# Kernel tuning notes

Hardware: AMD Instinct MI355X
Metric: run time of the kernel (lower is better)

Reference implementation:

```python
import jax, jax.numpy as jnp
import numpy as np

EPS = 1e-10


def setup_inputs() -> dict:
    key = jax.random.key(0)
    k1, k2, k3 = jax.random.split(key, 3)
    B, K, M, X, Y = 32, 4, 3, 256, 256
    predictions = jax.random.uniform(k1, (B, K, X, Y), dtype=jnp.float32)
    inputs = jax.random.normal(k2, (B, M, X, Y), dtype=jnp.float32)
    heart = jax.random.randint(k3, (B, 1, X, Y), 0, 2, dtype=jnp.int32)
    return {"predictions": predictions, "inputs": inputs, "heart": heart}


def reference(predictions, inputs, heart):
    # predictions: [B,K,X,Y] soft class maps; inputs: [B,M,X,Y]; heart: [B,1,X,Y] 0/1 ROI
    mask = (heart[:, 0] == 1).astype(predictions.dtype)            # [B,X,Y]
    n = jnp.sum(mask, axis=(-2, -1))                                # [B] masked pixel count
    pred = predictions * mask[:, None]                              # [B,K,X,Y] zero outside ROI
    # alpha[b,k] = mean of pred over masked pixels
    alpha = jnp.sum(pred, axis=(-2, -1)) / n[:, None]               # [B,K]
    s = jnp.sum(pred, axis=(-2, -1)) + EPS                          # [B,K]
    # weighted means mu[b,k,m] = sum(pred*inp)/ (sum(pred)+eps)
    mu = jnp.einsum('bkxy,bmxy->bkm', pred, inputs) / s[:, :, None]  # [B,K,M]
    diff = inputs[:, None] - mu[:, :, :, None, None]                 # [B,K,M,X,Y]
    var = jnp.einsum('bkmxy,bkxy->bkm', diff * diff, pred) / s[:, :, None] + EPS  # [B,K,M]
    # Gaussian pdf per (k,m), product over channels m (done in log-space, same math)
    v = var[:, :, :, None, None]
    log_pdf = -0.5 * jnp.log(2.0 * jnp.pi * v) - (diff * diff) / (2.0 * v)  # [B,K,M,X,Y]
    g = jnp.exp(jnp.sum(log_pdf, axis=2))                            # [B,K,X,Y] = prod_m pdf
    mix = jnp.sum(alpha[:, :, None, None] * g, axis=1)               # [B,X,Y]
    ll = jnp.log(mix + EPS)                                          # [B,X,Y]
    # mean of -log-likelihood over masked pixels per batch, then mean over batch
    per_b = -jnp.sum(mask * ll, axis=(-2, -1)) / n                   # [B]
    return jnp.mean(per_b)
```

## Files before the change

kernel.cpp:

```cpp
#include <hip/hip_runtime.h>

#define EPSF 1e-10f

constexpr int B = 32, K = 4, M = 3;
constexpr int NPIX = 256 * 256;
constexpr int BLOCKS_PER_B = 32;
constexpr int THREADS = 256;
constexpr int WAVES = THREADS / 64;
constexpr int CHUNKS = NPIX / (BLOCKS_PER_B * THREADS * 4);
constexpr int NVALS = 1 + K + 2 * K * M;

constexpr int OFF_PART1 = 0;
constexpr int OFF_PART2 = OFF_PART1 + B * BLOCKS_PER_B * NVALS;
constexpr int OFF_ALPHA = OFF_PART2 + B * BLOCKS_PER_B;
constexpr int OFF_MU    = OFF_ALPHA + B * K;
constexpr int OFF_IV    = OFF_MU + B * K * M;
constexpr int OFF_CST   = OFF_IV + B * K * M;
constexpr int OFF_NOUT  = OFF_CST + B * K;

__device__ __forceinline__ float wave_reduce(float v) {
    #pragma unroll
    for (int off = 32; off > 0; off >>= 1) v += __shfl_down(v, off, 64);
    return v;
}

__global__ __launch_bounds__(THREADS) void pass1_kernel(
    const float* __restrict__ pred, const float* __restrict__ xin,
    const int* __restrict__ heart, float* __restrict__ ws) {
    const int b  = blockIdx.x / BLOCKS_PER_B;
    const int cb = blockIdx.x % BLOCKS_PER_B;

    float nacc = 0.0f;
    float Wk[K] = {};
    float Pa[K][M] = {};
    float Qa[K][M] = {};

    #pragma unroll
    for (int it = 0; it < CHUNKS; ++it) {
        const int p0 = (((cb * CHUNKS + it) * THREADS) + threadIdx.x) * 4;

        const int4 h4 = *(const int4*)(heart + b * NPIX + p0);
        float mk[4];
        mk[0] = (h4.x == 1) ? 1.0f : 0.0f;
        mk[1] = (h4.y == 1) ? 1.0f : 0.0f;
        mk[2] = (h4.z == 1) ? 1.0f : 0.0f;
        mk[3] = (h4.w == 1) ? 1.0f : 0.0f;
        nacc += (mk[0] + mk[1]) + (mk[2] + mk[3]);

        float xv[M][4];
        #pragma unroll
        for (int m = 0; m < M; ++m) {
            float4 t = *(const float4*)(xin + (b * M + m) * NPIX + p0);
            xv[m][0] = t.x; xv[m][1] = t.y; xv[m][2] = t.z; xv[m][3] = t.w;
        }

        #pragma unroll
        for (int k = 0; k < K; ++k) {
            float4 pr = *(const float4*)(pred + (b * K + k) * NPIX + p0);
            float pm[4];
            pm[0] = pr.x * mk[0]; pm[1] = pr.y * mk[1];
            pm[2] = pr.z * mk[2]; pm[3] = pr.w * mk[3];
            Wk[k] += (pm[0] + pm[1]) + (pm[2] + pm[3]);
            #pragma unroll
            for (int m = 0; m < M; ++m) {
                #pragma unroll
                for (int j = 0; j < 4; ++j) {
                    float px = pm[j] * xv[m][j];
                    Pa[k][m] += px;
                    Qa[k][m] += px * xv[m][j];
                }
            }
        }
    }

    float vals[NVALS];
    vals[0] = nacc;
    #pragma unroll
    for (int k = 0; k < K; ++k) vals[1 + k] = Wk[k];
    #pragma unroll
    for (int k = 0; k < K; ++k)
        #pragma unroll
        for (int m = 0; m < M; ++m) {
            vals[1 + K + k * M + m]         = Pa[k][m];
            vals[1 + K + K * M + k * M + m] = Qa[k][m];
        }

    __shared__ float red[WAVES * NVALS];
    #pragma unroll
    for (int i = 0; i < NVALS; ++i) vals[i] = wave_reduce(vals[i]);
    const int wave = threadIdx.x >> 6;
    if ((threadIdx.x & 63) == 0) {
        #pragma unroll
        for (int i = 0; i < NVALS; ++i) red[wave * NVALS + i] = vals[i];
    }
    __syncthreads();
    const int i = threadIdx.x;
    if (i < NVALS) {
        float s = red[i];
        #pragma unroll
        for (int w = 1; w < WAVES; ++w) s += red[w * NVALS + i];
        ws[OFF_PART1 + (b * BLOCKS_PER_B + cb) * NVALS + i] = s;
    }
}

__global__ __launch_bounds__(B * K) void params_kernel(float* __restrict__ ws) {
    const int t = threadIdx.x;
    const int b = t / K;
    const int k = t % K;

    float n = 0.0f, W = 0.0f, P[M] = {}, Q[M] = {};
    for (int p = 0; p < BLOCKS_PER_B; ++p) {
        const float* base = ws + OFF_PART1 + (b * BLOCKS_PER_B + p) * NVALS;
        n += base[0];
        W += base[1 + k];
        #pragma unroll
        for (int m = 0; m < M; ++m) {
            P[m] += base[1 + K + k * M + m];
            Q[m] += base[1 + K + K * M + k * M + m];
        }
    }

    const float s = W + EPSF;
    ws[OFF_ALPHA + t] = W / n;
    if (k == 0) ws[OFF_NOUT + b] = n;
    float cst = 0.0f;
    #pragma unroll
    for (int m = 0; m < M; ++m) {
        const float mu = P[m] / s;
        const float var = (Q[m] - 2.0f * mu * P[m] + mu * mu * W) / s + EPSF;
        ws[OFF_MU + t * M + m] = mu;
        ws[OFF_IV + t * M + m] = 0.5f / var;
        cst -= 0.5f * logf(6.2831853071795864f * var);
    }
    ws[OFF_CST + t] = cst;
}

__global__ __launch_bounds__(THREADS) void pass2_kernel(
    const float* __restrict__ xin, const int* __restrict__ heart,
    float* __restrict__ ws) {
    const int b  = blockIdx.x / BLOCKS_PER_B;
    const int cb = blockIdx.x % BLOCKS_PER_B;

    float alpha[K], cst[K], mu[K][M], iv[K][M];
    #pragma unroll
    for (int k = 0; k < K; ++k) {
        alpha[k] = ws[OFF_ALPHA + b * K + k];
        cst[k]   = ws[OFF_CST + b * K + k];
        #pragma unroll
        for (int m = 0; m < M; ++m) {
            mu[k][m] = ws[OFF_MU + (b * K + k) * M + m];
            iv[k][m] = ws[OFF_IV + (b * K + k) * M + m];
        }
    }

    float acc = 0.0f;
    #pragma unroll
    for (int it = 0; it < CHUNKS; ++it) {
        const int p0 = (((cb * CHUNKS + it) * THREADS) + threadIdx.x) * 4;

        const int4 h4 = *(const int4*)(heart + b * NPIX + p0);
        int hv[4] = {h4.x, h4.y, h4.z, h4.w};

        float xv[M][4];
        #pragma unroll
        for (int m = 0; m < M; ++m) {
            float4 t = *(const float4*)(xin + (b * M + m) * NPIX + p0);
            xv[m][0] = t.x; xv[m][1] = t.y; xv[m][2] = t.z; xv[m][3] = t.w;
        }

        #pragma unroll
        for (int j = 0; j < 4; ++j) {
            float mix = EPSF;
            #pragma unroll
            for (int k = 0; k < K; ++k) {
                float lp = cst[k];
                #pragma unroll
                for (int m = 0; m < M; ++m) {
                    float d = xv[m][j] - mu[k][m];
                    lp -= d * d * iv[k][m];
                }
                mix += alpha[k] * __expf(lp);
            }
            float mask = (hv[j] == 1) ? 1.0f : 0.0f;
            acc += mask * __logf(mix);
        }
    }

    __shared__ float red[WAVES];
    acc = wave_reduce(acc);
    const int wave = threadIdx.x >> 6;
    if ((threadIdx.x & 63) == 0) red[wave] = acc;
    __syncthreads();
    if (threadIdx.x == 0) {
        float s = red[0];
        #pragma unroll
        for (int w = 1; w < WAVES; ++w) s += red[w];
        ws[OFF_PART2 + b * BLOCKS_PER_B + cb] = s;
    }
}

__global__ __launch_bounds__(64) void final_kernel(const float* __restrict__ ws,
                                                   float* __restrict__ out) {
    const int t = threadIdx.x;
    float val = 0.0f;
    if (t < B) {
        float s = 0.0f;
        for (int p = 0; p < BLOCKS_PER_B; ++p)
            s += ws[OFF_PART2 + t * BLOCKS_PER_B + p];
        val = -s / ws[OFF_NOUT + t];
    }
    val = wave_reduce(val);
    if (t == 0) out[0] = val / (float)B;
}

extern "C" void kernel_launch(void* const* d_in, const int* in_sizes, int n_in,
                              void* d_out, int out_size, void* d_ws, size_t ws_size,
                              hipStream_t stream) {
    const float* pred  = (const float*)d_in[0];
    const float* xin   = (const float*)d_in[1];
    const int*   heart = (const int*)d_in[2];
    float* out = (float*)d_out;
    float* ws  = (float*)d_ws;

    pass1_kernel<<<B * BLOCKS_PER_B, THREADS, 0, stream>>>(pred, xin, heart, ws);
    params_kernel<<<1, B * K, 0, stream>>>(ws);
    pass2_kernel<<<B * BLOCKS_PER_B, THREADS, 0, stream>>>(xin, heart, ws);
    final_kernel<<<1, 64, 0, stream>>>(ws, out);
}
```

Baseline: 113.3 us.

## Fuse all passes into one cooperative kernel with grid syncs and LDS-cached inputs

Replaces the four-kernel sequence with a single cooperative kernel that uses grid-wide syncs between the statistics pass, the per-batch parameter computation and the likelihood pass. Each block keeps its slice of inputs and the mask in shared memory (about 32 KB), so the second pass no longer re-reads inputs and heart from global memory. Every block redundantly reduces the per-batch partials to compute its own parameters, which removes the separate params and final launches. The cost is two grid barriers, higher LDS use that can limit occupancy for 1024 co-resident blocks, and a fallback to the old kernels if the cooperative launch fails.

```diff
diff --git a/kernel.cpp b/kernel.cpp
--- a/kernel.cpp
+++ b/kernel.cpp
@@ -1,22 +1,27 @@
 #include <hip/hip_runtime.h>
+#include <hip/hip_cooperative_groups.h>
+
+namespace cg = cooperative_groups;
 
 #define EPSF 1e-10f
 
 constexpr int B = 32, K = 4, M = 3;
 constexpr int NPIX = 256 * 256;
-constexpr int BLOCKS_PER_B = 32;
+constexpr int BPB = 32;
 constexpr int THREADS = 256;
 constexpr int WAVES = THREADS / 64;
-constexpr int CHUNKS = NPIX / (BLOCKS_PER_B * THREADS * 4);
+constexpr int PXB = NPIX / BPB;
+constexpr int CHUNKS = PXB / (THREADS * 4);
 constexpr int NVALS = 1 + K + 2 * K * M;
-
-constexpr int OFF_PART1 = 0;
-constexpr int OFF_PART2 = OFF_PART1 + B * BLOCKS_PER_B * NVALS;
-constexpr int OFF_ALPHA = OFF_PART2 + B * BLOCKS_PER_B;
+constexpr int PSTRIDE = 32;
+
+constexpr int OFF_P1 = 0;
+constexpr int OFF_LLP = OFF_P1 + B * BPB * PSTRIDE;
+constexpr int OFF_N  = OFF_LLP + B * BPB;
+constexpr int OFF_ALPHA = OFF_N + B;
 constexpr int OFF_MU    = OFF_ALPHA + B * K;
 constexpr int OFF_IV    = OFF_MU + B * K * M;
 constexpr int OFF_CST   = OFF_IV + B * K * M;
-constexpr int OFF_NOUT  = OFF_CST + B * K;
 
 __device__ __forceinline__ float wave_reduce(float v) {
     #pragma unroll
@@ -24,11 +29,17 @@
     return v;
 }
 
-__global__ __launch_bounds__(THREADS) void pass1_kernel(
+__global__ __launch_bounds__(THREADS, 4) void fused_kernel(
     const float* __restrict__ pred, const float* __restrict__ xin,
-    const int* __restrict__ heart, float* __restrict__ ws) {
-    const int b  = blockIdx.x / BLOCKS_PER_B;
-    const int cb = blockIdx.x % BLOCKS_PER_B;
+    const int* __restrict__ heart, float* __restrict__ ws, float* __restrict__ out) {
+    __shared__ float xs[M][PXB];
+    __shared__ float msk[PXB];
+    __shared__ float red[WAVES * NVALS];
+    __shared__ float par[K * 8];
+
+    const int b  = blockIdx.x / BPB;
+    const int cb = blockIdx.x % BPB;
+    const int tid = threadIdx.x;
 
     float nacc = 0.0f;
     float Wk[K] = {};
@@ -37,7 +48,8 @@
 
     #pragma unroll
     for (int it = 0; it < CHUNKS; ++it) {
-        const int p0 = (((cb * CHUNKS + it) * THREADS) + threadIdx.x) * 4;
+        const int li = (it * THREADS + tid) * 4;
+        const int p0 = cb * PXB + li;
 
         const int4 h4 = *(const int4*)(heart + b * NPIX + p0);
         float mk[4];
@@ -45,12 +57,14 @@
         mk[1] = (h4.y == 1) ? 1.0f : 0.0f;
         mk[2] = (h4.z == 1) ? 1.0f : 0.0f;
         mk[3] = (h4.w == 1) ? 1.0f : 0.0f;
+        *(float4*)&msk[li] = make_float4(mk[0], mk[1], mk[2], mk[3]);
         nacc += (mk[0] + mk[1]) + (mk[2] + mk[3]);
 
         float xv[M][4];
         #pragma unroll
         for (int m = 0; m < M; ++m) {
             float4 t = *(const float4*)(xin + (b * M + m) * NPIX + p0);
+            *(float4*)&xs[m][li] = t;
             xv[m][0] = t.x; xv[m][1] = t.y; xv[m][2] = t.z; xv[m][3] = t.w;
         }
 
@@ -84,90 +98,76 @@
             vals[1 + K + k * M + m]         = Pa[k][m];
             vals[1 + K + K * M + k * M + m] = Qa[k][m];
         }
-
-    __shared__ float red[WAVES * NVALS];
     #pragma unroll
     for (int i = 0; i < NVALS; ++i) vals[i] = wave_reduce(vals[i]);
-    const int wave = threadIdx.x >> 6;
-    if ((threadIdx.x & 63) == 0) {
+    const int wave = tid >> 6;
+    if ((tid & 63) == 0) {
         #pragma unroll
         for (int i = 0; i < NVALS; ++i) red[wave * NVALS + i] = vals[i];
     }
     __syncthreads();
-    const int i = threadIdx.x;
-    if (i < NVALS) {
-        float s = red[i];
-        #pragma unroll
-        for (int w = 1; w < WAVES; ++w) s += red[w * NVALS + i];
-        ws[OFF_PART1 + (b * BLOCKS_PER_B + cb) * NVALS + i] = s;
-    }
-}
-
-__global__ __launch_bounds__(B * K) void params_kernel(float* __restrict__ ws) {
-    const int t = threadIdx.x;
-    const int b = t / K;
-    const int k = t % K;
-
-    float n = 0.0f, W = 0.0f, P[M] = {}, Q[M] = {};
-    for (int p = 0; p < BLOCKS_PER_B; ++p) {
-        const float* base = ws + OFF_PART1 + (b * BLOCKS_PER_B + p) * NVALS;
-        n += base[0];
-        W += base[1 + k];
-        #pragma unroll
-        for (int m = 0; m < M; ++m) {
-            P[m] += base[1 + K + k * M + m];
-            Q[m] += base[1 + K + K * M + k * M + m];
-        }
-    }
-
-    const float s = W + EPSF;
-    ws[OFF_ALPHA + t] = W / n;
-    if (k == 0) ws[OFF_NOUT + b] = n;
-    float cst = 0.0f;
-    #pragma unroll
-    for (int m = 0; m < M; ++m) {
-        const float mu = P[m] / s;
-        const float var = (Q[m] - 2.0f * mu * P[m] + mu * mu * W) / s + EPSF;
-        ws[OFF_MU + t * M + m] = mu;
-        ws[OFF_IV + t * M + m] = 0.5f / var;
-        cst -= 0.5f * logf(6.2831853071795864f * var);
-    }
-    ws[OFF_CST + t] = cst;
-}
-
-__global__ __launch_bounds__(THREADS) void pass2_kernel(
-    const float* __restrict__ xin, const int* __restrict__ heart,
-    float* __restrict__ ws) {
-    const int b  = blockIdx.x / BLOCKS_PER_B;
-    const int cb = blockIdx.x % BLOCKS_PER_B;
+    if (tid < NVALS) {
+        float s = red[tid];
+        #pragma unroll
+        for (int w = 1; w < WAVES; ++w) s += red[w * NVALS + tid];
+        ws[OFF_P1 + (b * BPB + cb) * PSTRIDE + tid] = s;
+    }
+    __threadfence();
+    cg::this_grid().sync();
+
+    if (tid < K) {
+        const int k = tid;
+        float n = 0.0f, W = 0.0f, P[M] = {}, Q[M] = {};
+        for (int p = 0; p < BPB; ++p) {
+            const float* base = ws + OFF_P1 + (b * BPB + p) * PSTRIDE;
+            n += base[0];
+            W += base[1 + k];
+            #pragma unroll
+            for (int m = 0; m < M; ++m) {
+                P[m] += base[1 + K + k * M + m];
+                Q[m] += base[1 + K + K * M + k * M + m];
+            }
+        }
+        const float s = W + EPSF;
+        par[k * 8 + 0] = W / n;
+        float cst = 0.0f;
+        #pragma unroll
+        for (int m = 0; m < M; ++m) {
+            const float mu = P[m] / s;
+            const float var = (Q[m] - 2.0f * mu * P[m] + mu * mu * W) / s + EPSF;
+            par[k * 8 + 2 + m] = mu;
+            par[k * 8 + 5 + m] = 0.5f / var;
+            cst -= 0.5f * logf(6.2831853071795864f * var);
+        }
+        par[k * 8 + 1] = cst;
+        if (k == 0 && cb == 0) ws[OFF_N + b] = n;
+    }
+    __syncthreads();
 
     float alpha[K], cst[K], mu[K][M], iv[K][M];
     #pragma unroll
     for (int k = 0; k < K; ++k) {
-        alpha[k] = ws[OFF_ALPHA + b * K + k];
-        cst[k]   = ws[OFF_CST + b * K + k];
-        #pragma unroll
-        for (int m = 0; m < M; ++m) {
-            mu[k][m] = ws[OFF_MU + (b * K + k) * M + m];
-            iv[k][m] = ws[OFF_IV + (b * K + k) * M + m];
+        alpha[k] = par[k * 8 + 0];
+        cst[k]   = par[k * 8 + 1];
+        #pragma unroll
+        for (int m = 0; m < M; ++m) {
+            mu[k][m] = par[k * 8 + 2 + m];
+            iv[k][m] = par[k * 8 + 5 + m];
         }
     }
 
     float acc = 0.0f;
     #pragma unroll
     for (int it = 0; it < CHUNKS; ++it) {
-        const int p0 = (((cb * CHUNKS + it) * THREADS) + threadIdx.x) * 4;
-
-        const int4 h4 = *(const int4*)(heart + b * NPIX + p0);
-        int hv[4] = {h4.x, h4.y, h4.z, h4.w};
-
+        const int li = (it * THREADS + tid) * 4;
+        const float4 mk4 = *(const float4*)&msk[li];
+        const float mk[4] = {mk4.x, mk4.y, mk4.z, mk4.w};
         float xv[M][4];
         #pragma unroll
         for (int m = 0; m < M; ++m) {
-            float4 t = *(const float4*)(xin + (b * M + m) * NPIX + p0);
+            float4 t = *(const float4*)&xs[m][li];
             xv[m][0] = t.x; xv[m][1] = t.y; xv[m][2] = t.z; xv[m][3] = t.w;
         }
-
         #pragma unroll
         for (int j = 0; j < 4; ++j) {
             float mix = EPSF;
@@ -181,11 +181,179 @@
                 }
                 mix += alpha[k] * __expf(lp);
             }
-            float mask = (hv[j] == 1) ? 1.0f : 0.0f;
-            acc += mask * __logf(mix);
-        }
-    }
-
+            acc += mk[j] * __logf(mix);
+        }
+    }
+
+    __syncthreads();
+    acc = wave_reduce(acc);
+    if ((tid & 63) == 0) red[wave] = acc;
+    __syncthreads();
+    if (tid == 0) {
+        float s2 = red[0];
+        #pragma unroll
+        for (int w = 1; w < WAVES; ++w) s2 += red[w];
+        ws[OFF_LLP + b * BPB + cb] = s2;
+    }
+    __threadfence();
+    cg::this_grid().sync();
+
+    if (blockIdx.x == 0 && tid < 64) {
+        float val = 0.0f;
+        if (tid < B) {
+            float s = 0.0f;
+            for (int p = 0; p < BPB; ++p) s += ws[OFF_LLP + tid * BPB + p];
+            val = -s / ws[OFF_N + tid];
+        }
+        val = wave_reduce(val);
+        if (tid == 0) out[0] = val / (float)B;
+    }
+}
+
+__global__ __launch_bounds__(THREADS) void pass1_kernel(
+    const float* __restrict__ pred, const float* __restrict__ xin,
+    const int* __restrict__ heart, float* __restrict__ ws) {
+    const int b  = blockIdx.x / BPB;
+    const int cb = blockIdx.x % BPB;
+    float nacc = 0.0f;
+    float Wk[K] = {};
+    float Pa[K][M] = {};
+    float Qa[K][M] = {};
+    #pragma unroll
+    for (int it = 0; it < CHUNKS; ++it) {
+        const int p0 = cb * PXB + (it * THREADS + threadIdx.x) * 4;
+        const int4 h4 = *(const int4*)(heart + b * NPIX + p0);
+        float mk[4];
+        mk[0] = (h4.x == 1) ? 1.0f : 0.0f;
+        mk[1] = (h4.y == 1) ? 1.0f : 0.0f;
+        mk[2] = (h4.z == 1) ? 1.0f : 0.0f;
+        mk[3] = (h4.w == 1) ? 1.0f : 0.0f;
+        nacc += (mk[0] + mk[1]) + (mk[2] + mk[3]);
+        float xv[M][4];
+        #pragma unroll
+        for (int m = 0; m < M; ++m) {
+            float4 t = *(const float4*)(xin + (b * M + m) * NPIX + p0);
+            xv[m][0] = t.x; xv[m][1] = t.y; xv[m][2] = t.z; xv[m][3] = t.w;
+        }
+        #pragma unroll
+        for (int k = 0; k < K; ++k) {
+            float4 pr = *(const float4*)(pred + (b * K + k) * NPIX + p0);
+            float pm[4];
+            pm[0] = pr.x * mk[0]; pm[1] = pr.y * mk[1];
+            pm[2] = pr.z * mk[2]; pm[3] = pr.w * mk[3];
+            Wk[k] += (pm[0] + pm[1]) + (pm[2] + pm[3]);
+            #pragma unroll
+            for (int m = 0; m < M; ++m)
+                #pragma unroll
+                for (int j = 0; j < 4; ++j) {
+                    float px = pm[j] * xv[m][j];
+                    Pa[k][m] += px;
+                    Qa[k][m] += px * xv[m][j];
+                }
+        }
+    }
+    float vals[NVALS];
+    vals[0] = nacc;
+    #pragma unroll
+    for (int k = 0; k < K; ++k) vals[1 + k] = Wk[k];
+    #pragma unroll
+    for (int k = 0; k < K; ++k)
+        #pragma unroll
+        for (int m = 0; m < M; ++m) {
+            vals[1 + K + k * M + m]         = Pa[k][m];
+            vals[1 + K + K * M + k * M + m] = Qa[k][m];
+        }
+    __shared__ float red[WAVES * NVALS];
+    #pragma unroll
+    for (int i = 0; i < NVALS; ++i) vals[i] = wave_reduce(vals[i]);
+    const int wave = threadIdx.x >> 6;
+    if ((threadIdx.x & 63) == 0) {
+        #pragma unroll
+        for (int i = 0; i < NVALS; ++i) red[wave * NVALS + i] = vals[i];
+    }
+    __syncthreads();
+    if (threadIdx.x < NVALS) {
+        float s = red[threadIdx.x];
+        #pragma unroll
+        for (int w = 1; w < WAVES; ++w) s += red[w * NVALS + threadIdx.x];
+        ws[OFF_P1 + (b * BPB + cb) * PSTRIDE + threadIdx.x] = s;
+    }
+}
+
+__global__ __launch_bounds__(B * K) void params_kernel(float* __restrict__ ws) {
+    const int t = threadIdx.x;
+    const int b = t / K;
+    const int k = t % K;
+    float n = 0.0f, W = 0.0f, P[M] = {}, Q[M] = {};
+    for (int p = 0; p < BPB; ++p) {
+        const float* base = ws + OFF_P1 + (b * BPB + p) * PSTRIDE;
+        n += base[0];
+        W += base[1 + k];
+        #pragma unroll
+        for (int m = 0; m < M; ++m) {
+            P[m] += base[1 + K + k * M + m];
+            Q[m] += base[1 + K + K * M + k * M + m];
+        }
+    }
+    const float s = W + EPSF;
+    ws[OFF_ALPHA + t] = W / n;
+    if (k == 0) ws[OFF_N + b] = n;
+    float cst = 0.0f;
+    #pragma unroll
+    for (int m = 0; m < M; ++m) {
+        const float mu = P[m] / s;
+        const float var = (Q[m] - 2.0f * mu * P[m] + mu * mu * W) / s + EPSF;
+        ws[OFF_MU + t * M + m] = mu;
+        ws[OFF_IV + t * M + m] = 0.5f / var;
+        cst -= 0.5f * logf(6.2831853071795864f * var);
+    }
+    ws[OFF_CST + t] = cst;
+}
+
+__global__ __launch_bounds__(THREADS) void pass2_kernel(
+    const float* __restrict__ xin, const int* __restrict__ heart,
+    float* __restrict__ ws) {
+    const int b  = blockIdx.x / BPB;
+    const int cb = blockIdx.x % BPB;
+    float alpha[K], cst[K], mu[K][M], iv[K][M];
+    #pragma unroll
+    for (int k = 0; k < K; ++k) {
+        alpha[k] = ws[OFF_ALPHA + b * K + k];
+        cst[k]   = ws[OFF_CST + b * K + k];
+        #pragma unroll
+        for (int m = 0; m < M; ++m) {
+            mu[k][m] = ws[OFF_MU + (b * K + k) * M + m];
+            iv[k][m] = ws[OFF_IV + (b * K + k) * M + m];
+        }
+    }
+    float acc = 0.0f;
+    #pragma unroll
+    for (int it = 0; it < CHUNKS; ++it) {
+        const int p0 = cb * PXB + (it * THREADS + threadIdx.x) * 4;
+        const int4 h4 = *(const int4*)(heart + b * NPIX + p0);
+        int hv[4] = {h4.x, h4.y, h4.z, h4.w};
+        float xv[M][4];
+        #pragma unroll
+        for (int m = 0; m < M; ++m) {
+            float4 t = *(const float4*)(xin + (b * M + m) * NPIX + p0);
+            xv[m][0] = t.x; xv[m][1] = t.y; xv[m][2] = t.z; xv[m][3] = t.w;
+        }
+        #pragma unroll
+        for (int j = 0; j < 4; ++j) {
+            float mix = EPSF;
+            #pragma unroll
+            for (int k = 0; k < K; ++k) {
+                float lp = cst[k];
+                #pragma unroll
+                for (int m = 0; m < M; ++m) {
+                    float d = xv[m][j] - mu[k][m];
+                    lp -= d * d * iv[k][m];
+                }
+                mix += alpha[k] * __expf(lp);
+            }
+            acc += ((hv[j] == 1) ? 1.0f : 0.0f) * __logf(mix);
+        }
+    }
     __shared__ float red[WAVES];
     acc = wave_reduce(acc);
     const int wave = threadIdx.x >> 6;
@@ -195,7 +363,7 @@
         float s = red[0];
         #pragma unroll
         for (int w = 1; w < WAVES; ++w) s += red[w];
-        ws[OFF_PART2 + b * BLOCKS_PER_B + cb] = s;
+        ws[OFF_LLP + b * BPB + cb] = s;
     }
 }
 
@@ -205,9 +373,8 @@
     float val = 0.0f;
     if (t < B) {
         float s = 0.0f;
-        for (int p = 0; p < BLOCKS_PER_B; ++p)
-            s += ws[OFF_PART2 + t * BLOCKS_PER_B + p];
-        val = -s / ws[OFF_NOUT + t];
+        for (int p = 0; p < BPB; ++p) s += ws[OFF_LLP + t * BPB + p];
+        val = -s / ws[OFF_N + t];
     }
     val = wave_reduce(val);
     if (t == 0) out[0] = val / (float)B;
@@ -222,8 +389,15 @@
     float* out = (float*)d_out;
     float* ws  = (float*)d_ws;
 
-    pass1_kernel<<<B * BLOCKS_PER_B, THREADS, 0, stream>>>(pred, xin, heart, ws);
-    params_kernel<<<1, B * K, 0, stream>>>(ws);
-    pass2_kernel<<<B * BLOCKS_PER_B, THREADS, 0, stream>>>(xin, heart, ws);
-    final_kernel<<<1, 64, 0, stream>>>(ws, out);
-}
+    void* args[] = {(void*)&pred, (void*)&xin, (void*)&heart, (void*)&ws, (void*)&out};
+    hipError_t e = hipLaunchCooperativeKernel((const void*)fused_kernel,
+                                              dim3(B * BPB), dim3(THREADS),
+                                              args, 0, stream);
+    if (e != hipSuccess) {
+        (void)hipGetLastError();
+        pass1_kernel<<<B * BPB, THREADS, 0, stream>>>(pred, xin, heart, ws);
+        params_kernel<<<1, B * K, 0, stream>>>(ws);
+        pass2_kernel<<<B * BPB, THREADS, 0, stream>>>(xin, heart, ws);
+        final_kernel<<<1, 64, 0, stream>>>(ws, out);
+    }
+}
```

Result: slower. 424.3 us (+274.5%).
